# Kernel optimization log

Hardware: AMD Instinct MI355X
Metric: run time of the kernel (lower is better)

## Reference

```python
import jax, jax.numpy as jnp
import numpy as np

MSE_WEIGHT = 1.0
PHYSICS_WEIGHT = 0.1
VAR_IDX = np.array([2, 1, 0, 3, 4])
VAR_W = np.array([0.5, 0.15, 0.15, 0.1, 0.1], dtype=np.float32)
TEMP_IDX = np.array([5, 7, 8, 9, 11])
TEMP_W = 0.1
TEMP_THRESH = 5.0


def setup_inputs() -> dict:
    key = jax.random.key(0)
    k1, k2, k3, k4, k5 = jax.random.split(key, 5)
    B, S, W, D = 524288, 4, 8, 16
    return {
        "pred": jax.random.normal(k1, (B, S, D), dtype=jnp.float32),
        "target": jax.random.normal(k2, (B, S, D), dtype=jnp.float32),
        "input_sequence": jax.random.normal(k3, (B, W, D), dtype=jnp.float32),
        "scale": jax.random.uniform(k4, (D,), dtype=jnp.float32, minval=0.5, maxval=2.0),
        "mean": jax.random.normal(k5, (D,), dtype=jnp.float32),
    }


def reference(pred, target, input_sequence, scale, mean):
    B, S, D = pred.shape
    # step weights: 1/(k+1), normalized
    step_w = 1.0 / (jnp.arange(S, dtype=jnp.float32) + 1.0)
    step_w = step_w / jnp.sum(step_w)

    # --- weighted per-variable MSE (gradients flow through pred/target) ---
    var_idx = jnp.asarray(VAR_IDX)
    var_w = jnp.asarray(VAR_W)
    diff2 = (pred[:, :, var_idx] - target[:, :, var_idx]) ** 2  # [B, S, 5]
    mse_per_step = jnp.einsum("bsv,v->s", diff2, var_w) / B      # [S]
    mse_loss = jnp.dot(step_w, mse_per_step)

    # --- physics terms on detached, de-normalized states ---
    pred_sg = jax.lax.stop_gradient(pred)
    prev = jnp.concatenate(
        [jax.lax.stop_gradient(input_sequence[:, -1:, :]), pred_sg[:, :-1, :]], axis=1
    )  # [B, S, D]
    pd = pred_sg * scale + mean   # inverse_transform (StandardScaler)
    pv = prev * scale + mean

    air, water = pd[:, :, 3], pd[:, :, 4]
    heat_balance = jnp.mean((air - water) ** 2, axis=0) / (jnp.mean(air ** 2, axis=0) + 1e-6)  # [S]

    frost_dec = jax.nn.relu(pv[:, :, 2] - pd[:, :, 2])
    frost_mono = jnp.mean(frost_dec ** 2, axis=0)  # [S]

    press_dec = jax.nn.relu(pv[:, :, 0] - pd[:, :, 0]) * 0.5
    press_growth = jnp.mean(press_dec ** 2, axis=0)  # [S]

    tidx = jnp.asarray(TEMP_IDX)
    temp_diff = jnp.abs(pd[:, :, tidx] - pv[:, :, tidx])            # [B, S, 5]
    temp_pen = TEMP_W * jnp.sum(jnp.mean(jax.nn.relu(temp_diff - TEMP_THRESH) ** 2, axis=0), axis=-1)  # [S]

    physics_per_step = heat_balance + frost_mono + press_growth + temp_pen  # [S]
    physics_loss = jnp.dot(step_w, physics_per_step)

    return MSE_WEIGHT * mse_loss + PHYSICS_WEIGHT * physics_loss
```

## Files before the change

### kernel.cpp

```cpp
#include <hip/hip_runtime.h>

#define B_TOTAL 524288
#define TILE_B 128
#define NBLK (B_TOTAL / TILE_B)
#define NTHR 256


__global__ __launch_bounds__(NTHR) void loss_partial(
    const float* __restrict__ pred,
    const float* __restrict__ target,
    const float* __restrict__ inseq,
    const float* __restrict__ scale,
    const float* __restrict__ mean,
    float* __restrict__ partials)
{
    __shared__ float4 sp[TILE_B * 16];
    __shared__ float4 st[TILE_B * 8];
    __shared__ float red[4][10];

    const int tid = threadIdx.x;
    const size_t tile0 = (size_t)blockIdx.x * TILE_B;

    const float4* prg = reinterpret_cast<const float4*>(pred) + tile0 * 16;
    const float4* tgg = reinterpret_cast<const float4*>(target) + tile0 * 16;

#pragma unroll
    for (int i = 0; i < 8; ++i) {
        int j = i * NTHR + tid;
        sp[j ^ ((j >> 4) & 7)] = prg[j];
    }
#pragma unroll
    for (int i = 0; i < 4; ++i) {
        int j = i * NTHR + tid;
        st[j ^ ((j >> 3) & 7)] = tgg[((j >> 1) << 2) | (j & 1)];
    }

    const int b = tid >> 1;
    const int shalf = tid & 1;

    float pv0 = 0.f, pv2 = 0.f, pv5 = 0.f, pv7 = 0.f, pv8 = 0.f, pv9 = 0.f, pv11 = 0.f;
    if (!shalf) {
        const float4* iq = reinterpret_cast<const float4*>(inseq + (tile0 + (size_t)b) * 128 + 112);
        float4 q0 = iq[0], q1 = iq[1], q2 = iq[2];
        pv0 = q0.x; pv2 = q0.z; pv5 = q1.y; pv7 = q1.w;
        pv8 = q2.x; pv9 = q2.y; pv11 = q2.w;
    }

    const float sc0 = scale[0], sc2 = scale[2], sc3 = scale[3], sc4 = scale[4];
    const float sc5 = scale[5], sc7 = scale[7], sc8 = scale[8], sc9 = scale[9], sc11 = scale[11];
    const float mn3 = mean[3], mn4 = mean[4];

    __syncthreads();

    auto ldp = [&](int s, int w) -> float4 {
        int i = (b << 4) + (s << 2) + w;
        return sp[i ^ ((i >> 4) & 7)];
    };
    auto ldt = [&](int s, int h) -> float4 {
        int i = (b << 3) + (s << 1) + h;
        return st[i ^ ((i >> 3) & 7)];
    };

    const int sA = shalf ? 2 : 0;
    if (shalf) {
        float4 q0 = ldp(1, 0), q1 = ldp(1, 1), q2 = ldp(1, 2);
        pv0 = q0.x; pv2 = q0.z; pv5 = q1.y; pv7 = q1.w;
        pv8 = q2.x; pv9 = q2.y; pv11 = q2.w;
    }

    const float swA = shalf ? 0.16f : 0.48f;
    const float swB = shalf ? 0.12f : 0.24f;

    float acc_mse = 0.f, acc_rest = 0.f;
    float hnA, hdA, hnB, hdB;

    auto cell = [&](int s, float sw, float& hn, float& hd) {
        float4 p0 = ldp(s, 0), p1 = ldp(s, 1), p2 = ldp(s, 2);
        float4 t0 = ldt(s, 0), t1 = ldt(s, 1);
        float d0 = p0.x - t0.x, d1 = p0.y - t0.y, d2 = p0.z - t0.z;
        float d3 = p0.w - t0.w, d4 = p1.x - t1.x;
        acc_mse += sw * (0.15f * d0 * d0 + 0.15f * d1 * d1 + 0.5f * d2 * d2 +
                         0.1f * d3 * d3 + 0.1f * d4 * d4);
        float air = p0.w * sc3 + mn3;
        float water = p1.x * sc4 + mn4;
        float h = air - water;
        hn = h * h;
        hd = air * air;
        float fr = fmaxf((pv2 - p0.z) * sc2, 0.f);
        float pg = fmaxf((pv0 - p0.x) * sc0, 0.f) * 0.5f;
        float rest = fr * fr + pg * pg;
        float t5 = fmaxf(fabsf(p1.y - pv5) * sc5 - 5.f, 0.f);
        float t7 = fmaxf(fabsf(p1.w - pv7) * sc7 - 5.f, 0.f);
        float t8 = fmaxf(fabsf(p2.x - pv8) * sc8 - 5.f, 0.f);
        float t9 = fmaxf(fabsf(p2.y - pv9) * sc9 - 5.f, 0.f);
        float t11 = fmaxf(fabsf(p2.w - pv11) * sc11 - 5.f, 0.f);
        rest += 0.1f * (t5 * t5 + t7 * t7 + t8 * t8 + t9 * t9 + t11 * t11);
        acc_rest += sw * rest;
        pv0 = p0.x; pv2 = p0.z; pv5 = p1.y; pv7 = p1.w;
        pv8 = p2.x; pv9 = p2.y; pv11 = p2.w;
    };

    cell(sA,     swA, hnA, hdA);
    cell(sA + 1, swB, hnB, hdB);

    float vals[10];
    vals[0] = acc_mse;
    vals[1] = acc_rest;
    vals[2] = shalf ? 0.f : hnA;
    vals[3] = shalf ? 0.f : hnB;
    vals[4] = shalf ? hnA : 0.f;
    vals[5] = shalf ? hnB : 0.f;
    vals[6] = shalf ? 0.f : hdA;
    vals[7] = shalf ? 0.f : hdB;
    vals[8] = shalf ? hdA : 0.f;
    vals[9] = shalf ? hdB : 0.f;

    const int lane = tid & 63;
    const int wave = tid >> 6;
#pragma unroll
    for (int i = 0; i < 10; ++i) {
        float v = vals[i];
#pragma unroll
        for (int off = 32; off; off >>= 1) v += __shfl_down(v, off, 64);
        if (lane == 0) red[wave][i] = v;
    }
    __syncthreads();
    if (tid < 10) {
        partials[tid * NBLK + blockIdx.x] =
            red[0][tid] + red[1][tid] + red[2][tid] + red[3][tid];
    }
}

__global__ __launch_bounds__(640) void loss_final(
    const float* __restrict__ partials,
    float* __restrict__ out)
{
    __shared__ float tot[10];
    const int t = threadIdx.x;
    const int c = t >> 6;
    const int lane = t & 63;

    float v = 0.f;
#pragma unroll
    for (int i = 0; i < NBLK / 64; ++i)
        v += partials[(size_t)c * NBLK + i * 64 + lane];
#pragma unroll
    for (int off = 32; off; off >>= 1) v += __shfl_down(v, off, 64);
    if (lane == 0) tot[c] = v;
    __syncthreads();

    if (t == 0) {
        const float stepw[4] = {0.48f, 0.24f, 0.16f, 0.12f};
        const float invB = 1.0f / (float)B_TOTAL;
        float mse = tot[0] * invB;
        float phys = tot[1] * invB;
#pragma unroll
        for (int s = 0; s < 4; ++s) {
            float num = tot[2 + s] * invB;
            float den = tot[6 + s] * invB + 1e-6f;
            phys += stepw[s] * (num / den);
        }
        out[0] = mse + 0.1f * phys;
    }
}

extern "C" void kernel_launch(void* const* d_in, const int* in_sizes, int n_in,
                              void* d_out, int out_size, void* d_ws, size_t ws_size,
                              hipStream_t stream) {
    const float* pred   = (const float*)d_in[0];
    const float* target = (const float*)d_in[1];
    const float* inseq  = (const float*)d_in[2];
    const float* scale  = (const float*)d_in[3];
    const float* mean   = (const float*)d_in[4];
    float* out = (float*)d_out;
    float* partials = (float*)d_ws;

    loss_partial<<<NBLK, NTHR, 0, stream>>>(pred, target, inseq, scale, mean, partials);
    loss_final<<<1, 640, 0, stream>>>(partials, out);
}
```

Measured before the change: 65.22 us.

## Assign one thread per (batch, step) cell and load only used pred columns

```diff
diff --git a/kernel.cpp b/kernel.cpp
--- a/kernel.cpp
+++ b/kernel.cpp
@@ -3,10 +3,10 @@
 #define B_TOTAL 524288
 #define TILE_B 128
 #define NBLK (B_TOTAL / TILE_B)
-#define NTHR 256
+#define NTHR 512
 
 
-__global__ __launch_bounds__(NTHR) void loss_partial(
+__global__ __launch_bounds__(NTHR, 8) void loss_partial(
     const float* __restrict__ pred,
     const float* __restrict__ target,
     const float* __restrict__ inseq,
@@ -14,9 +14,8 @@
     const float* __restrict__ mean,
     float* __restrict__ partials)
 {
-    __shared__ float4 sp[TILE_B * 16];
+    __shared__ float4 sp[TILE_B * 12];
     __shared__ float4 st[TILE_B * 8];
-    __shared__ float red[4][10];
 
     const int tid = threadIdx.x;
     const size_t tile0 = (size_t)blockIdx.x * TILE_B;
@@ -25,21 +24,22 @@
     const float4* tgg = reinterpret_cast<const float4*>(target) + tile0 * 16;
 
 #pragma unroll
-    for (int i = 0; i < 8; ++i) {
-        int j = i * NTHR + tid;
-        sp[j ^ ((j >> 4) & 7)] = prg[j];
+    for (int it = 0; it < 3; ++it) {
+        int j = it * NTHR + tid;
+        int row = j / 3, k = j - row * 3;
+        sp[j ^ ((j >> 3) & 7)] = prg[row * 4 + k];
     }
 #pragma unroll
-    for (int i = 0; i < 4; ++i) {
-        int j = i * NTHR + tid;
+    for (int it = 0; it < 2; ++it) {
+        int j = it * NTHR + tid;
         st[j ^ ((j >> 3) & 7)] = tgg[((j >> 1) << 2) | (j & 1)];
     }
 
-    const int b = tid >> 1;
-    const int shalf = tid & 1;
+    const int b = tid >> 2;
+    const int s = tid & 3;
 
     float pv0 = 0.f, pv2 = 0.f, pv5 = 0.f, pv7 = 0.f, pv8 = 0.f, pv9 = 0.f, pv11 = 0.f;
-    if (!shalf) {
+    if (s == 0) {
         const float4* iq = reinterpret_cast<const float4*>(inseq + (tile0 + (size_t)b) * 128 + 112);
         float4 q0 = iq[0], q1 = iq[1], q2 = iq[2];
         pv0 = q0.x; pv2 = q0.z; pv5 = q1.y; pv7 = q1.w;
@@ -49,85 +49,76 @@
     const float sc0 = scale[0], sc2 = scale[2], sc3 = scale[3], sc4 = scale[4];
     const float sc5 = scale[5], sc7 = scale[7], sc8 = scale[8], sc9 = scale[9], sc11 = scale[11];
     const float mn3 = mean[3], mn4 = mean[4];
+    const float sw = (s == 0) ? 0.48f : (s == 1) ? 0.24f : (s == 2) ? 0.16f : 0.12f;
 
     __syncthreads();
 
-    auto ldp = [&](int s, int w) -> float4 {
-        int i = (b << 4) + (s << 2) + w;
-        return sp[i ^ ((i >> 4) & 7)];
+    auto ldp = [&](int row, int w) -> float4 {
+        int i = row * 3 + w;
+        return sp[i ^ ((i >> 3) & 7)];
     };
-    auto ldt = [&](int s, int h) -> float4 {
-        int i = (b << 3) + (s << 1) + h;
+    auto ldt = [&](int row, int h) -> float4 {
+        int i = row * 2 + h;
         return st[i ^ ((i >> 3) & 7)];
     };
 
-    const int sA = shalf ? 2 : 0;
-    if (shalf) {
-        float4 q0 = ldp(1, 0), q1 = ldp(1, 1), q2 = ldp(1, 2);
+    const int row = b * 4 + s;
+    if (s != 0) {
+        float4 q0 = ldp(row - 1, 0), q1 = ldp(row - 1, 1), q2 = ldp(row - 1, 2);
         pv0 = q0.x; pv2 = q0.z; pv5 = q1.y; pv7 = q1.w;
         pv8 = q2.x; pv9 = q2.y; pv11 = q2.w;
     }
 
-    const float swA = shalf ? 0.16f : 0.48f;
-    const float swB = shalf ? 0.12f : 0.24f;
+    float4 p0 = ldp(row, 0), p1 = ldp(row, 1), p2 = ldp(row, 2);
+    float4 t0 = ldt(row, 0), t1 = ldt(row, 1);
 
-    float acc_mse = 0.f, acc_rest = 0.f;
-    float hnA, hdA, hnB, hdB;
+    float d0 = p0.x - t0.x, d1 = p0.y - t0.y, d2 = p0.z - t0.z;
+    float d3 = p0.w - t0.w, d4 = p1.x - t1.x;
+    float acc_mse = sw * (0.15f * d0 * d0 + 0.15f * d1 * d1 + 0.5f * d2 * d2 +
+                          0.1f * d3 * d3 + 0.1f * d4 * d4);
 
-    auto cell = [&](int s, float sw, float& hn, float& hd) {
-        float4 p0 = ldp(s, 0), p1 = ldp(s, 1), p2 = ldp(s, 2);
-        float4 t0 = ldt(s, 0), t1 = ldt(s, 1);
-        float d0 = p0.x - t0.x, d1 = p0.y - t0.y, d2 = p0.z - t0.z;
-        float d3 = p0.w - t0.w, d4 = p1.x - t1.x;
-        acc_mse += sw * (0.15f * d0 * d0 + 0.15f * d1 * d1 + 0.5f * d2 * d2 +
-                         0.1f * d3 * d3 + 0.1f * d4 * d4);
-        float air = p0.w * sc3 + mn3;
-        float water = p1.x * sc4 + mn4;
-        float h = air - water;
-        hn = h * h;
-        hd = air * air;
-        float fr = fmaxf((pv2 - p0.z) * sc2, 0.f);
-        float pg = fmaxf((pv0 - p0.x) * sc0, 0.f) * 0.5f;
-        float rest = fr * fr + pg * pg;
-        float t5 = fmaxf(fabsf(p1.y - pv5) * sc5 - 5.f, 0.f);
-        float t7 = fmaxf(fabsf(p1.w - pv7) * sc7 - 5.f, 0.f);
-        float t8 = fmaxf(fabsf(p2.x - pv8) * sc8 - 5.f, 0.f);
-        float t9 = fmaxf(fabsf(p2.y - pv9) * sc9 - 5.f, 0.f);
-        float t11 = fmaxf(fabsf(p2.w - pv11) * sc11 - 5.f, 0.f);
-        rest += 0.1f * (t5 * t5 + t7 * t7 + t8 * t8 + t9 * t9 + t11 * t11);
-        acc_rest += sw * rest;
-        pv0 = p0.x; pv2 = p0.z; pv5 = p1.y; pv7 = p1.w;
-        pv8 = p2.x; pv9 = p2.y; pv11 = p2.w;
-    };
+    float air = p0.w * sc3 + mn3;
+    float water = p1.x * sc4 + mn4;
+    float hdf = air - water;
+    float hn = hdf * hdf;
+    float hd = air * air;
 
-    cell(sA,     swA, hnA, hdA);
-    cell(sA + 1, swB, hnB, hdB);
+    float fr = fmaxf((pv2 - p0.z) * sc2, 0.f);
+    float pg = fmaxf((pv0 - p0.x) * sc0, 0.f) * 0.5f;
+    float rest = fr * fr + pg * pg;
+    float t5 = fmaxf(fabsf(p1.y - pv5) * sc5 - 5.f, 0.f);
+    float t7 = fmaxf(fabsf(p1.w - pv7) * sc7 - 5.f, 0.f);
+    float t8 = fmaxf(fabsf(p2.x - pv8) * sc8 - 5.f, 0.f);
+    float t9 = fmaxf(fabsf(p2.y - pv9) * sc9 - 5.f, 0.f);
+    float t11 = fmaxf(fabsf(p2.w - pv11) * sc11 - 5.f, 0.f);
+    rest += 0.1f * (t5 * t5 + t7 * t7 + t8 * t8 + t9 * t9 + t11 * t11);
+    float acc_rest = sw * rest;
 
-    float vals[10];
-    vals[0] = acc_mse;
-    vals[1] = acc_rest;
-    vals[2] = shalf ? 0.f : hnA;
-    vals[3] = shalf ? 0.f : hnB;
-    vals[4] = shalf ? hnA : 0.f;
-    vals[5] = shalf ? hnB : 0.f;
-    vals[6] = shalf ? 0.f : hdA;
-    vals[7] = shalf ? 0.f : hdB;
-    vals[8] = shalf ? hdA : 0.f;
-    vals[9] = shalf ? hdB : 0.f;
+    __syncthreads();
 
     const int lane = tid & 63;
     const int wave = tid >> 6;
 #pragma unroll
-    for (int i = 0; i < 10; ++i) {
-        float v = vals[i];
+    for (int off = 1; off < 64; off <<= 1) {
+        acc_mse  += __shfl_xor(acc_mse, off, 64);
+        acc_rest += __shfl_xor(acc_rest, off, 64);
+    }
 #pragma unroll
-        for (int off = 32; off; off >>= 1) v += __shfl_down(v, off, 64);
-        if (lane == 0) red[wave][i] = v;
+    for (int off = 4; off < 64; off <<= 1) {
+        hn += __shfl_xor(hn, off, 64);
+        hd += __shfl_xor(hd, off, 64);
     }
+
+    float* red = reinterpret_cast<float*>(st);
+    if (lane == 0) { red[wave * 10 + 0] = acc_mse; red[wave * 10 + 1] = acc_rest; }
+    if (lane < 4)  { red[wave * 10 + 2 + lane] = hn; red[wave * 10 + 6 + lane] = hd; }
     __syncthreads();
+
     if (tid < 10) {
-        partials[tid * NBLK + blockIdx.x] =
-            red[0][tid] + red[1][tid] + red[2][tid] + red[3][tid];
+        float v = 0.f;
+#pragma unroll
+        for (int w = 0; w < 8; ++w) v += red[w * 10 + tid];
+        partials[tid * NBLK + blockIdx.x] = v;
     }
 }
 
```

Measured after the change: 62.20 us. 1.05x faster.
